# Kernel tuning notes

Measured on AMD Instinct MI355X. Metric: run time of the kernel, lower is better.

The kernel has to match this reference:

```python
import jax, jax.numpy as jnp
import numpy as np

B, N, C, H = 8, 4096, 256, 8
D = C // H
HID = 4 * C
EPS = 1e-5

def _ln(x, w, b):
    mu = jnp.mean(x, axis=-1, keepdims=True)
    var = jnp.var(x, axis=-1, keepdims=True)
    return (x - mu) * jax.lax.rsqrt(var + EPS) * w + b

def setup_inputs() -> dict:
    key = jax.random.key(0)
    ks = jax.random.split(key, 16)
    s = lambda k, shp, scale=0.02: jax.random.normal(k, shp, dtype=jnp.float32) * scale
    return {
        "input_": jax.random.normal(ks[0], (B, N, C), dtype=jnp.float32),
        "prev_state": jax.random.normal(ks[1], (B, N, C), dtype=jnp.float32),
        "pos_embed": jax.random.normal(ks[2], (1, N, C), dtype=jnp.float32),
        "norm1_w": jnp.ones((C,), jnp.float32), "norm1_b": jnp.zeros((C,), jnp.float32),
        "norm2_w": jnp.ones((C,), jnp.float32), "norm2_b": jnp.zeros((C,), jnp.float32),
        "norm3_w": jnp.ones((C,), jnp.float32), "norm3_b": jnp.zeros((C,), jnp.float32),
        "qkv_input_w": s(ks[3], (3 * C, C)),
        "qkv_state_w": s(ks[4], (3 * C, C)),
        "proj_w": s(ks[5], (C, C)), "proj_b": jnp.zeros((C,), jnp.float32),
        "gate_w": s(ks[6], (C, 2 * C)), "gate_b": jnp.zeros((C,), jnp.float32),
        "fc1_w": s(ks[7], (HID, C)), "fc1_b": jnp.zeros((HID,), jnp.float32),
        "fc2_w": s(ks[8], (C, HID)), "fc2_b": jnp.zeros((C,), jnp.float32),
    }

def reference(input_, prev_state, pos_embed,
              norm1_w, norm1_b, norm2_w, norm2_b, norm3_w, norm3_b,
              qkv_input_w, qkv_state_w, proj_w, proj_b,
              gate_w, gate_b, fc1_w, fc1_b, fc2_w, fc2_b):
    input_pos = input_ + pos_embed
    x_ln = _ln(input_pos, norm1_w, norm1_b)
    s_ln = _ln(prev_state, norm2_w, norm2_b)
    # fused QKV from input and state; torch Linear: x @ W.T
    qkv_i = (x_ln @ qkv_input_w.T).reshape(B, N, 3, H, D).transpose(2, 0, 3, 1, 4)
    qkv_s = (s_ln @ qkv_state_w.T).reshape(B, N, 3, H, D).transpose(2, 0, 3, 1, 4)
    q = qkv_i[0] + qkv_s[0]  # [B,H,N,D]
    k = qkv_i[1] + qkv_s[1]
    v = qkv_i[2] + qkv_s[2]
    phi_q = jax.nn.elu(q) + 1.0
    phi_k = jax.nn.elu(k) + 1.0
    # (phi_q @ phi_k^T) @ v reordered associatively to O(N*D^2)
    kv = jnp.einsum('bhnd,bhne->bhde', phi_k, v)        # [B,H,D,D]
    attn = jnp.einsum('bhnd,bhde->bhne', phi_q, kv)     # [B,H,N,D]
    attn = attn.transpose(0, 2, 1, 3).reshape(B, N, C)
    attn = attn @ proj_w.T + proj_b
    output = input_pos + attn
    stacked = jnp.concatenate([input_, prev_state], axis=2)
    update = jax.nn.sigmoid(stacked @ gate_w.T + gate_b)
    new_state = prev_state * (1.0 - update) + attn * update
    h = _ln(output, norm3_w, norm3_b)
    h = jax.nn.gelu(h @ fc1_w.T + fc1_b, approximate=False) @ fc2_w.T + fc2_b
    output = output + h
    return (output, new_state)
```

## Files before the change

### kernel.cpp

```cpp
#include <hip/hip_runtime.h>
#include <cmath>

typedef unsigned short u16;
typedef __attribute__((ext_vector_type(8))) short short8;
typedef __attribute__((ext_vector_type(4))) float f32x4;
typedef __attribute__((ext_vector_type(4))) u16 u16x4;

__device__ __forceinline__ float b2f(u16 u) {
    unsigned x = ((unsigned)u) << 16;
    return __builtin_bit_cast(float, x);
}
__device__ __forceinline__ u16 f2b(float f) {
    unsigned x = __builtin_bit_cast(unsigned, f);
    unsigned r = (x + 0x7fffu + ((x >> 16) & 1u)) >> 16;
    return (u16)r;
}
__device__ __forceinline__ float loadx(const void* p, size_t i, int f32) {
    return f32 ? ((const float*)p)[i] : b2f(((const u16*)p)[i]);
}
__device__ __forceinline__ void stage8f(u16* dst, const void* src, size_t eoff) {
    const f32x4* s = (const f32x4*)((const float*)src + eoff);
    f32x4 a = s[0], b = s[1];
    uint4 p;
    p.x = (unsigned)f2b(a[0]) | ((unsigned)f2b(a[1]) << 16);
    p.y = (unsigned)f2b(a[2]) | ((unsigned)f2b(a[3]) << 16);
    p.z = (unsigned)f2b(b[0]) | ((unsigned)f2b(b[1]) << 16);
    p.w = (unsigned)f2b(b[2]) | ((unsigned)f2b(b[3]) << 16);
    *(uint4*)dst = p;
}
__device__ __forceinline__ void gl_lds16(const void* g, void* l) {
    __builtin_amdgcn_global_load_lds(
        (const __attribute__((address_space(1))) void*)g,
        (__attribute__((address_space(3))) void*)l, 16, 0, 0);
}
__device__ __forceinline__ float gelu_f(float x) {
    float y = 0.7978845608028654f * (x + 0.044715f * x * x * x);
    float e = __expf(2.f * y);
    float t = 1.f - 2.f / (e + 1.f);
    return 0.5f * x * (1.f + t);
}

#define BB 8
#define NN 4096
#define CC 256
#define HH 8
#define DD 32
#define HID 1024
#define MTOK (BB*NN)
#define TOKEL ((size_t)MTOK*CC)

#define WS_INPUT_POS 0u
#define WS_PHIQ   16777216u
#define WS_PHIK   33554432u
#define WS_V      50331648u
#define WS_XLN    67108864u
#define WS_SLN    83886080u
#define WS_OUTPRE 100663296u
#define WS_FLAG   117440512u

__global__ __launch_bounds__(64) void detect_kernel(const u16* __restrict__ in0,
                                                    int* __restrict__ flag)
{
    int t = threadIdx.x;
    u16 w = in0[2 * t];
    int e = (w >> 7) & 0xFF;
    int bad = (e < 64 || e > 192) ? 1 : 0;
    unsigned long long m = __ballot(bad);
    if (t == 0) *flag = (__popcll(m) > 8) ? 1 : 0;
}

__global__ __launch_bounds__(256) void prep_kernel(
    const void* __restrict__ inp, const void* __restrict__ prev,
    const void* __restrict__ pos,
    const void* __restrict__ w1, const void* __restrict__ b1,
    const void* __restrict__ w2, const void* __restrict__ b2,
    u16* __restrict__ input_pos, u16* __restrict__ x_ln, u16* __restrict__ s_ln,
    const int* __restrict__ flagp)
{
    const int f32 = *flagp;
    const int m = blockIdx.x;
    const int c = threadIdx.x;
    const int n = m & (NN - 1);
    const size_t idx = (size_t)m * CC + c;

    __shared__ float red[8];

    float ip = loadx(inp, idx, f32) + loadx(pos, (size_t)n * CC + c, f32);
    float s = ip, s2 = ip * ip;
    #pragma unroll
    for (int o = 32; o; o >>= 1) { s += __shfl_down(s, o, 64); s2 += __shfl_down(s2, o, 64); }
    if ((threadIdx.x & 63) == 0) { int w6 = threadIdx.x >> 6; red[w6] = s; red[4 + w6] = s2; }
    __syncthreads();
    float mu  = (red[0] + red[1] + red[2] + red[3]) * (1.f / 256.f);
    float var = (red[4] + red[5] + red[6] + red[7]) * (1.f / 256.f) - mu * mu;
    float rs = rsqrtf(var + 1e-5f);
    input_pos[idx] = f2b(ip);
    x_ln[idx] = f2b((ip - mu) * rs * loadx(w1, c, f32) + loadx(b1, c, f32));
    __syncthreads();

    float pv = loadx(prev, idx, f32);
    s = pv; s2 = pv * pv;
    #pragma unroll
    for (int o = 32; o; o >>= 1) { s += __shfl_down(s, o, 64); s2 += __shfl_down(s2, o, 64); }
    if ((threadIdx.x & 63) == 0) { int w6 = threadIdx.x >> 6; red[w6] = s; red[4 + w6] = s2; }
    __syncthreads();
    mu  = (red[0] + red[1] + red[2] + red[3]) * (1.f / 256.f);
    var = (red[4] + red[5] + red[6] + red[7]) * (1.f / 256.f) - mu * mu;
    rs = rsqrtf(var + 1e-5f);
    s_ln[idx] = f2b((pv - mu) * rs * loadx(w2, c, f32) + loadx(b2, c, f32));
}

__global__ __launch_bounds__(256) void ln3_kernel(
    const u16* __restrict__ op, const void* __restrict__ w,
    const void* __restrict__ b, u16* __restrict__ out, const int* __restrict__ flagp)
{
    const int f32 = *flagp;
    const size_t m = blockIdx.x;
    const int c = threadIdx.x;
    const size_t idx = m * CC + c;
    __shared__ float red[8];
    float x = b2f(op[idx]);
    float s = x, s2 = x * x;
    #pragma unroll
    for (int o = 32; o; o >>= 1) { s += __shfl_down(s, o, 64); s2 += __shfl_down(s2, o, 64); }
    if ((threadIdx.x & 63) == 0) { int w6 = threadIdx.x >> 6; red[w6] = s; red[4 + w6] = s2; }
    __syncthreads();
    float mu  = (red[0] + red[1] + red[2] + red[3]) * (1.f / 256.f);
    float var = (red[4] + red[5] + red[6] + red[7]) * (1.f / 256.f) - mu * mu;
    out[idx] = f2b((x - mu) * rsqrtf(var + 1e-5f) * loadx(w, c, f32) + loadx(b, c, f32));
}

__global__ __launch_bounds__(64) void kv_mfma(
    const u16* __restrict__ phik_t, const u16* __restrict__ v_t,
    float* __restrict__ kvout)
{
    const int bh = blockIdx.x;
    const int k0 = blockIdx.y * 256;
    const int lane = threadIdx.x;
    const int quad = lane >> 4, lr = lane & 15;

    const u16* A = phik_t + (size_t)bh * DD * NN;
    const u16* W = v_t    + (size_t)bh * DD * NN;

    f32x4 acc[2][2];
    #pragma unroll
    for (int i = 0; i < 2; ++i)
        #pragma unroll
        for (int j = 0; j < 2; ++j) { f32x4 z = {0.f,0.f,0.f,0.f}; acc[i][j] = z; }

    for (int kk = k0; kk < k0 + 256; kk += 32) {
        short8 a0 = *(const short8*)(A + (size_t)lr * NN + kk + quad * 8);
        short8 a1 = *(const short8*)(A + (size_t)(16 + lr) * NN + kk + quad * 8);
        short8 w0 = *(const short8*)(W + (size_t)lr * NN + kk + quad * 8);
        short8 w1 = *(const short8*)(W + (size_t)(16 + lr) * NN + kk + quad * 8);
        acc[0][0] = __builtin_amdgcn_mfma_f32_16x16x32_bf16(a0, w0, acc[0][0], 0, 0, 0);
        acc[0][1] = __builtin_amdgcn_mfma_f32_16x16x32_bf16(a0, w1, acc[0][1], 0, 0, 0);
        acc[1][0] = __builtin_amdgcn_mfma_f32_16x16x32_bf16(a1, w0, acc[1][0], 0, 0, 0);
        acc[1][1] = __builtin_amdgcn_mfma_f32_16x16x32_bf16(a1, w1, acc[1][1], 0, 0, 0);
    }
    float* base = kvout + (size_t)bh * (DD * DD);
    #pragma unroll
    for (int i = 0; i < 2; ++i)
        #pragma unroll
        for (int j = 0; j < 2; ++j)
            #pragma unroll
            for (int r = 0; r < 4; ++r)
                atomicAdd(base + (i * 16 + quad * 4 + r) * DD + j * 16 + lr, acc[i][j][r]);
}

__global__ __launch_bounds__(256) void attn_mfma(
    const u16* __restrict__ phiq, const float* __restrict__ kv,
    u16* __restrict__ attn_tok)
{
    const int bh = blockIdx.x;
    const int b = bh >> 3, h = bh & 7;
    const int wv = threadIdx.x >> 6, lane = threadIdx.x & 63;
    const int quad = lane >> 4, lr = lane & 15;

    const float* kvb = kv + (size_t)bh * (DD * DD);
    short8 bf0, bf1;
    #pragma unroll
    for (int j = 0; j < 8; ++j) {
        int d = quad * 8 + j;
        bf0[j] = (short)f2b(kvb[d * DD + lr]);
        bf1[j] = (short)f2b(kvb[d * DD + 16 + lr]);
    }

    const u16* qb = phiq + (size_t)bh * NN * DD;
    const int n0 = blockIdx.y * 512 + wv * 128;
    #pragma unroll
    for (int t = 0; t < 8; ++t) {
        const int nt = n0 + t * 16;
        short8 af = *(const short8*)(qb + (size_t)(nt + lr) * DD + quad * 8);
        f32x4 c0 = {0.f,0.f,0.f,0.f}, c1 = {0.f,0.f,0.f,0.f};
        c0 = __builtin_amdgcn_mfma_f32_16x16x32_bf16(af, bf0, c0, 0, 0, 0);
        c1 = __builtin_amdgcn_mfma_f32_16x16x32_bf16(af, bf1, c1, 0, 0, 0);
        size_t base = ((size_t)b * NN + nt + quad * 4) * CC + h * DD;
        #pragma unroll
        for (int r = 0; r < 4; ++r) {
            attn_tok[base + (size_t)r * CC + lr]      = f2b(c0[r]);
            attn_tok[base + (size_t)r * CC + 16 + lr] = f2b(c1[r]);
        }
    }
}

#define BM 128
#define BN 128
#define BK 32
#define LDT 32

template <int MODE, int RAWA>
__global__ __launch_bounds__(256) void gemm_bt(
    const void* __restrict__ A1, const void* __restrict__ A2,
    const void* __restrict__ W1, const void* __restrict__ W2,
    int lda, int ldw, int K, int Ksplit, int wcol2,
    const void* __restrict__ bias,
    u16* __restrict__ o0, u16* __restrict__ o1,
    const u16* __restrict__ xa, const void* __restrict__ xr,
    void* __restrict__ oraw, const int* __restrict__ flagp)
{
    __shared__ u16 ash[BM * LDT];
    __shared__ u16 bsh[BN * LDT];

    const int f32 = *flagp;
    const int af32 = RAWA ? f32 : 0;

    const int tid = threadIdx.x;
    const int lane = tid & 63;
    const int wv = tid >> 6;
    const int wm = wv >> 1, wn = wv & 1;
    const int quad = lane >> 4, lr = lane & 15;

    const bool swp = (MODE == 0) ? (blockIdx.x < 2) : true;

    f32x4 acc[4][4];
    #pragma unroll
    for (int i = 0; i < 4; ++i)
        #pragma unroll
        for (int j = 0; j < 4; ++j) { f32x4 z = {0.f,0.f,0.f,0.f}; acc[i][j] = z; }

    const size_t arow0 = (size_t)blockIdx.y * BM;
    const size_t wrow0 = (size_t)blockIdx.x * BN;

    const int srow = lane >> 2;
    const int skc  = (lane & 3) << 3;

    for (int k0 = 0; k0 < K; k0 += BK) {
        const void* As; const void* Ws; int ka, kw;
        if (k0 < Ksplit) { As = A1; Ws = W1; ka = k0;          kw = k0; }
        else             { As = A2; Ws = W2; ka = k0 - Ksplit; kw = k0 - Ksplit + wcol2; }

        if (!af32) {
            const u16* ga = (const u16*)As + (arow0 + wv * 32 + srow) * (size_t)lda + ka + skc;
            u16* la = ash + (wv * 32) * LDT;
            gl_lds16(ga, la);
            gl_lds16(ga + (size_t)16 * lda, la + 16 * LDT);
        } else {
            #pragma unroll
            for (int half = 0; half < 2; ++half) {
                int row = wv * 32 + half * 16 + srow;
                stage8f(ash + row * LDT + skc, As, (arow0 + row) * (size_t)lda + ka + skc);
            }
        }
        if (!f32) {
            const u16* gw = (const u16*)Ws + (wrow0 + wv * 32 + srow) * (size_t)ldw + kw + skc;
            u16* lb = bsh + (wv * 32) * LDT;
            gl_lds16(gw, lb);
            gl_lds16(gw + (size_t)16 * ldw, lb + 16 * LDT);
        } else {
            #pragma unroll
            for (int half = 0; half < 2; ++half) {
                int row = wv * 32 + half * 16 + srow;
                stage8f(bsh + row * LDT + skc, Ws, (wrow0 + row) * (size_t)ldw + kw + skc);
            }
        }
        __syncthreads();

        short8 af[4], bf[4];
        #pragma unroll
        for (int i = 0; i < 4; ++i)
            af[i] = *(const short8*)(ash + (wm * 64 + i * 16 + lr) * LDT + quad * 8);
        #pragma unroll
        for (int j = 0; j < 4; ++j)
            bf[j] = *(const short8*)(bsh + (wn * 64 + j * 16 + lr) * LDT + quad * 8);
        if (swp) {
            #pragma unroll
            for (int i = 0; i < 4; ++i)
                #pragma unroll
                for (int j = 0; j < 4; ++j)
                    acc[i][j] = __builtin_amdgcn_mfma_f32_16x16x32_bf16(bf[j], af[i], acc[i][j], 0, 0, 0);
        } else {
            #pragma unroll
            for (int i = 0; i < 4; ++i)
                #pragma unroll
                for (int j = 0; j < 4; ++j)
                    acc[i][j] = __builtin_amdgcn_mfma_f32_16x16x32_bf16(af[i], bf[j], acc[i][j], 0, 0, 0);
        }
        __syncthreads();
    }

    const int mbase = blockIdx.y * BM + wm * 64;
    const int nbase = blockIdx.x * BN + wn * 64;
    constexpr int LDOUT = (MODE == 3) ? HID : CC;

    #pragma unroll
    for (int i = 0; i < 4; ++i) {
        #pragma unroll
        for (int j = 0; j < 4; ++j) {
            if (MODE == 0) {
                if (swp) {
                    const int m = mbase + i * 16 + lr;
                    const int b = m >> 12, n = m & (NN - 1);
                    const int c0 = nbase + j * 16 + quad * 4;
                    const int h = c0 >> 5, d0 = c0 & 31;
                    u16x4 p;
                    #pragma unroll
                    for (int r = 0; r < 4; ++r) {
                        float v = acc[i][j][r];
                        p[r] = f2b((v > 0.f) ? (v + 1.f) : __expf(v));
                    }
                    *(u16x4*)(o0 + (((size_t)b * HH + h) * NN + n) * DD + d0) = p;
                } else {
                    const int c = nbase + j * 16 + lr;
                    const int which = c >> 8, rem = c & 255, h = rem >> 5, d = rem & 31;
                    const int m0 = mbase + i * 16 + quad * 4;
                    const int b = m0 >> 12, n0i = m0 & (NN - 1);
                    u16x4 p;
                    #pragma unroll
                    for (int r = 0; r < 4; ++r) {
                        float v = acc[i][j][r];
                        if (which == 1) v = (v > 0.f) ? (v + 1.f) : __expf(v);
                        p[r] = f2b(v);
                    }
                    u16* dst = o0 + (size_t)which * TOKEL;
                    *(u16x4*)(dst + (((size_t)b * HH + h) * DD + d) * NN + n0i) = p;
                }
            } else {
                const int m = mbase + i * 16 + lr;
                const int c0 = nbase + j * 16 + quad * 4;
                const size_t idx0 = (size_t)m * LDOUT + c0;
                float bias4[4];
                if (f32) {
                    f32x4 t = *(const f32x4*)((const float*)bias + c0);
                    #pragma unroll
                    for (int r = 0; r < 4; ++r) bias4[r] = t[r];
                } else {
                    u16x4 t = *(const u16x4*)((const u16*)bias + c0);
                    #pragma unroll
                    for (int r = 0; r < 4; ++r) bias4[r] = b2f(t[r]);
                }
                if (MODE == 1) {
                    u16x4 xa4 = *(const u16x4*)(xa + idx0);
                    u16x4 po, pr;
                    #pragma unroll
                    for (int r = 0; r < 4; ++r) {
                        float val = acc[i][j][r] + bias4[r];
                        po[r] = f2b(val);
                        pr[r] = f2b(b2f(xa4[r]) + val);
                    }
                    *(u16x4*)(o0 + idx0) = po;
                    *(u16x4*)(o1 + idx0) = pr;
                } else if (MODE == 2) {
                    u16x4 ap4 = *(const u16x4*)(xa + idx0);
                    float res[4];
                    if (f32) {
                        f32x4 pv = *(const f32x4*)((const float*)xr + idx0);
                        #pragma unroll
                        for (int r = 0; r < 4; ++r) {
                            float u = 1.f / (1.f + __expf(-(acc[i][j][r] + bias4[r])));
                            res[r] = pv[r] * (1.f - u) + b2f(ap4[r]) * u;
                        }
                        f32x4 o; o[0]=res[0]; o[1]=res[1]; o[2]=res[2]; o[3]=res[3];
                        *(f32x4*)((float*)oraw + TOKEL + idx0) = o;
                    } else {
                        u16x4 pv = *(const u16x4*)((const u16*)xr + idx0);
                        u16x4 o;
                        #pragma unroll
                        for (int r = 0; r < 4; ++r) {
                            float u = 1.f / (1.f + __expf(-(acc[i][j][r] + bias4[r])));
                            o[r] = f2b(b2f(pv[r]) * (1.f - u) + b2f(ap4[r]) * u);
                        }
                        *(u16x4*)((u16*)oraw + TOKEL + idx0) = o;
                    }
                } else if (MODE == 3) {
                    u16x4 p;
                    #pragma unroll
                    for (int r = 0; r < 4; ++r)
                        p[r] = f2b(gelu_f(acc[i][j][r] + bias4[r]));
                    *(u16x4*)(o0 + idx0) = p;
                } else {
                    u16x4 xa4 = *(const u16x4*)(xa + idx0);
                    if (f32) {
                        f32x4 o;
                        #pragma unroll
                        for (int r = 0; r < 4; ++r)
                            o[r] = b2f(xa4[r]) + acc[i][j][r] + bias4[r];
                        *(f32x4*)((float*)oraw + idx0) = o;
                    } else {
                        u16x4 o;
                        #pragma unroll
                        for (int r = 0; r < 4; ++r)
                            o[r] = f2b(b2f(xa4[r]) + acc[i][j][r] + bias4[r]);
                        *(u16x4*)((u16*)oraw + idx0) = o;
                    }
                }
            }
        }
    }
}

extern "C" void kernel_launch(void* const* d_in, const int* in_sizes, int n_in,
                              void* d_out, int out_size, void* d_ws, size_t ws_size,
                              hipStream_t stream)
{
    const void* input_ = d_in[0];
    const void* prev   = d_in[1];
    const void* pos    = d_in[2];
    const void* n1w = d_in[3];  const void* n1b = d_in[4];
    const void* n2w = d_in[5];  const void* n2b = d_in[6];
    const void* n3w = d_in[7];  const void* n3b = d_in[8];
    const void* qkvi = d_in[9]; const void* qkvs = d_in[10];
    const void* projw = d_in[11]; const void* projb = d_in[12];
    const void* gatew = d_in[13]; const void* gateb = d_in[14];
    const void* fc1w = d_in[15]; const void* fc1b = d_in[16];
    const void* fc2w = d_in[17]; const void* fc2b = d_in[18];

    char* ws = (char*)d_ws;
    u16* input_pos = (u16*)(ws + WS_INPUT_POS);
    u16* phiq  = (u16*)(ws + WS_PHIQ);
    u16* phikt = (u16*)(ws + WS_PHIK);
    u16* vt    = (u16*)(ws + WS_V);
    u16* x_ln = (u16*)(ws + WS_XLN);
    u16* s_ln = (u16*)(ws + WS_SLN);
    u16* attn_tok = x_ln;
    u16* attn_proj = phikt;
    float* kvf = (float*)(ws + WS_SLN);
    u16* ln3o = s_ln;
    u16* outpre = (u16*)(ws + WS_OUTPRE);
    u16* h1 = (u16*)(ws + WS_INPUT_POS);
    int* flagp = (int*)(ws + WS_FLAG);

    detect_kernel<<<1, 64, 0, stream>>>((const u16*)input_, flagp);
    prep_kernel<<<MTOK, 256, 0, stream>>>(input_, prev, pos, n1w, n1b, n2w, n2b,
                                          input_pos, x_ln, s_ln, flagp);
    gemm_bt<0, 0><<<dim3(3 * CC / BN, MTOK / BM), 256, 0, stream>>>(
        x_ln, s_ln, qkvi, qkvs, CC, CC, 2 * CC, CC, 0, nullptr,
        phiq, nullptr, nullptr, nullptr, nullptr, flagp);
    hipMemsetAsync((void*)kvf, 0, BB * HH * DD * DD * sizeof(float), stream);
    kv_mfma<<<dim3(BB * HH, 16), 64, 0, stream>>>(phikt, vt, kvf);
    attn_mfma<<<dim3(BB * HH, NN / 512), 256, 0, stream>>>(phiq, kvf, attn_tok);
    gemm_bt<1, 0><<<dim3(CC / BN, MTOK / BM), 256, 0, stream>>>(
        attn_tok, attn_tok, projw, projw, CC, CC, CC, CC, 0, projb,
        attn_proj, outpre, input_pos, nullptr, nullptr, flagp);
    gemm_bt<2, 1><<<dim3(CC / BN, MTOK / BM), 256, 0, stream>>>(
        input_, prev, gatew, gatew, CC, 2 * CC, 2 * CC, CC, CC, gateb,
        nullptr, nullptr, attn_proj, prev, d_out, flagp);
    ln3_kernel<<<MTOK, 256, 0, stream>>>(outpre, n3w, n3b, ln3o, flagp);
    gemm_bt<3, 0><<<dim3(HID / BN, MTOK / BM), 256, 0, stream>>>(
        ln3o, ln3o, fc1w, fc1w, CC, CC, CC, CC, 0, fc1b,
        h1, nullptr, nullptr, nullptr, nullptr, flagp);
    gemm_bt<4, 0><<<dim3(CC / BN, MTOK / BM), 256, 0, stream>>>(
        h1, h1, fc2w, fc2w, HID, HID, HID, HID, 0, fc2b,
        nullptr, nullptr, outpre, nullptr, d_out, flagp);
}
```

Measured before the change: 501.2 us.

## Pre-convert weights and raw inputs to bf16, relayout LDS tiles, remap workgroups per XCD

Adds a kernel that converts all weights and biases to bf16 once per call into device globals. The prep kernel now also writes bf16 copies of input and prev_state, so every GEMM, including the gate GEMM, can stage A and W through direct global-to-LDS loads instead of the fp32 convert-and-store path. The LDS tiles move to a k-group-major layout that changes the access pattern for the load and MFMA fragment reads. Workgroup IDs are remapped round-robin across 8 chunks, apparently to keep neighbouring tiles on the same XCD for L2 reuse. The cost is an extra launch and extra bf16 writes of both 8M-element tensors.

```diff
diff --git a/kernel.cpp b/kernel.cpp
--- a/kernel.cpp
+++ b/kernel.cpp
@@ -17,16 +17,6 @@
 }
 __device__ __forceinline__ float loadx(const void* p, size_t i, int f32) {
     return f32 ? ((const float*)p)[i] : b2f(((const u16*)p)[i]);
-}
-__device__ __forceinline__ void stage8f(u16* dst, const void* src, size_t eoff) {
-    const f32x4* s = (const f32x4*)((const float*)src + eoff);
-    f32x4 a = s[0], b = s[1];
-    uint4 p;
-    p.x = (unsigned)f2b(a[0]) | ((unsigned)f2b(a[1]) << 16);
-    p.y = (unsigned)f2b(a[2]) | ((unsigned)f2b(a[3]) << 16);
-    p.z = (unsigned)f2b(b[0]) | ((unsigned)f2b(b[1]) << 16);
-    p.w = (unsigned)f2b(b[2]) | ((unsigned)f2b(b[3]) << 16);
-    *(uint4*)dst = p;
 }
 __device__ __forceinline__ void gl_lds16(const void* g, void* l) {
     __builtin_amdgcn_global_load_lds(
@@ -48,6 +38,7 @@
 #define HID 1024
 #define MTOK (BB*NN)
 #define TOKEL ((size_t)MTOK*CC)
+#define TOKELC 8388608
 
 #define WS_INPUT_POS 0u
 #define WS_PHIQ   16777216u
@@ -58,6 +49,22 @@
 #define WS_OUTPRE 100663296u
 #define WS_FLAG   117440512u
 
+#define OFF_QKVI  0u
+#define OFF_QKVS  196608u
+#define OFF_PROJW 393216u
+#define OFF_GATEW 458752u
+#define OFF_FC1W  589824u
+#define OFF_FC2W  851968u
+#define OFF_PROJB 1114112u
+#define OFF_GATEB 1114368u
+#define OFF_FC1B  1114624u
+#define OFF_FC2B  1115648u
+#define WTOT      1115904u
+
+__device__ __attribute__((aligned(16))) u16 g_wb[WTOT];
+__device__ __attribute__((aligned(16))) u16 g_inb[TOKELC];
+__device__ __attribute__((aligned(16))) u16 g_prevb[TOKELC];
+
 __global__ __launch_bounds__(64) void detect_kernel(const u16* __restrict__ in0,
                                                     int* __restrict__ flag)
 {
@@ -67,6 +74,28 @@
     int bad = (e < 64 || e > 192) ? 1 : 0;
     unsigned long long m = __ballot(bad);
     if (t == 0) *flag = (__popcll(m) > 8) ? 1 : 0;
+}
+
+__global__ __launch_bounds__(256) void wconv_kernel(
+    const void* qkvi, const void* qkvs, const void* projw, const void* gatew,
+    const void* fc1w, const void* fc2w, const void* projb, const void* gateb,
+    const void* fc1b, const void* fc2b, const int* __restrict__ flagp)
+{
+    const int f32 = *flagp;
+    unsigned i = blockIdx.x * 256 + threadIdx.x;
+    if (i >= WTOT) return;
+    const void* src; unsigned off;
+    if      (i < OFF_QKVS)  { src = qkvi;  off = OFF_QKVI; }
+    else if (i < OFF_PROJW) { src = qkvs;  off = OFF_QKVS; }
+    else if (i < OFF_GATEW) { src = projw; off = OFF_PROJW; }
+    else if (i < OFF_FC1W)  { src = gatew; off = OFF_GATEW; }
+    else if (i < OFF_FC2W)  { src = fc1w;  off = OFF_FC1W; }
+    else if (i < OFF_PROJB) { src = fc2w;  off = OFF_FC2W; }
+    else if (i < OFF_GATEB) { src = projb; off = OFF_PROJB; }
+    else if (i < OFF_FC1B)  { src = gateb; off = OFF_GATEB; }
+    else if (i < OFF_FC2B)  { src = fc1b;  off = OFF_FC1B; }
+    else                    { src = fc2b;  off = OFF_FC2B; }
+    g_wb[i] = f2b(loadx(src, i - off, f32));
 }
 
 __global__ __launch_bounds__(256) void prep_kernel(
@@ -85,7 +114,9 @@
 
     __shared__ float red[8];
 
-    float ip = loadx(inp, idx, f32) + loadx(pos, (size_t)n * CC + c, f32);
+    float inr = loadx(inp, idx, f32);
+    float ip = inr + loadx(pos, (size_t)n * CC + c, f32);
+    g_inb[idx] = f2b(inr);
     float s = ip, s2 = ip * ip;
     #pragma unroll
     for (int o = 32; o; o >>= 1) { s += __shfl_down(s, o, 64); s2 += __shfl_down(s2, o, 64); }
@@ -99,6 +130,7 @@
     __syncthreads();
 
     float pv = loadx(prev, idx, f32);
+    g_prevb[idx] = f2b(pv);
     s = pv; s2 = pv * pv;
     #pragma unroll
     for (int o = 32; o; o >>= 1) { s += __shfl_down(s, o, 64); s2 += __shfl_down(s2, o, 64); }
@@ -207,23 +239,36 @@
 #define BM 128
 #define BN 128
 #define BK 32
-#define LDT 32
-
-template <int MODE, int RAWA>
+
+template <int MODE>
 __global__ __launch_bounds__(256) void gemm_bt(
-    const void* __restrict__ A1, const void* __restrict__ A2,
-    const void* __restrict__ W1, const void* __restrict__ W2,
+    const u16* __restrict__ A1in, const u16* __restrict__ A2in,
     int lda, int ldw, int K, int Ksplit, int wcol2,
-    const void* __restrict__ bias,
     u16* __restrict__ o0, u16* __restrict__ o1,
     const u16* __restrict__ xa, const void* __restrict__ xr,
     void* __restrict__ oraw, const int* __restrict__ flagp)
 {
-    __shared__ u16 ash[BM * LDT];
-    __shared__ u16 bsh[BN * LDT];
-
-    const int f32 = *flagp;
-    const int af32 = RAWA ? f32 : 0;
+    __shared__ __attribute__((aligned(16))) u16 ash[BM * BK];
+    __shared__ __attribute__((aligned(16))) u16 bsh[BN * BK];
+
+    const int f32 = (MODE == 2 || MODE == 4) ? *flagp : 0;
+
+    const u16* W1; const u16* W2; const u16* bias = nullptr;
+    if (MODE == 0)      { W1 = g_wb + OFF_QKVI; W2 = g_wb + OFF_QKVS; }
+    else if (MODE == 1) { W1 = W2 = g_wb + OFF_PROJW; bias = g_wb + OFF_PROJB; }
+    else if (MODE == 2) { W1 = W2 = g_wb + OFF_GATEW; bias = g_wb + OFF_GATEB; }
+    else if (MODE == 3) { W1 = W2 = g_wb + OFF_FC1W;  bias = g_wb + OFF_FC1B; }
+    else                { W1 = W2 = g_wb + OFF_FC2W;  bias = g_wb + OFF_FC2B; }
+    const u16* A1 = (MODE == 2) ? g_inb   : A1in;
+    const u16* A2 = (MODE == 2) ? g_prevb : A2in;
+
+    const int gx = gridDim.x;
+    const int nwg = gx * (int)gridDim.y;
+    const int hw = blockIdx.y * gx + blockIdx.x;
+    const int qq = nwg >> 3, rr = nwg & 7;
+    const int xc = hw & 7, pp = hw >> 3;
+    const int nid = (xc < rr ? xc * (qq + 1) : rr * (qq + 1) + (xc - rr) * qq) + pp;
+    const int bx = nid % gx, by = nid / gx;
 
     const int tid = threadIdx.x;
     const int lane = tid & 63;
@@ -231,7 +276,7 @@
     const int wm = wv >> 1, wn = wv & 1;
     const int quad = lane >> 4, lr = lane & 15;
 
-    const bool swp = (MODE == 0) ? (blockIdx.x < 2) : true;
+    const bool swp = (MODE == 0) ? (bx < 2) : true;
 
     f32x4 acc[4][4];
     #pragma unroll
@@ -239,50 +284,38 @@
         #pragma unroll
         for (int j = 0; j < 4; ++j) { f32x4 z = {0.f,0.f,0.f,0.f}; acc[i][j] = z; }
 
-    const size_t arow0 = (size_t)blockIdx.y * BM;
-    const size_t wrow0 = (size_t)blockIdx.x * BN;
-
-    const int srow = lane >> 2;
-    const int skc  = (lane & 3) << 3;
+    const size_t arow0 = (size_t)by * BM;
+    const size_t wrow0 = (size_t)bx * BN;
+
+    const int srow = lane & 31;
+    const int sg   = (lane >> 5) << 3;
 
     for (int k0 = 0; k0 < K; k0 += BK) {
-        const void* As; const void* Ws; int ka, kw;
+        const u16* As; const u16* Ws; int ka, kw;
         if (k0 < Ksplit) { As = A1; Ws = W1; ka = k0;          kw = k0; }
         else             { As = A2; Ws = W2; ka = k0 - Ksplit; kw = k0 - Ksplit + wcol2; }
 
-        if (!af32) {
-            const u16* ga = (const u16*)As + (arow0 + wv * 32 + srow) * (size_t)lda + ka + skc;
-            u16* la = ash + (wv * 32) * LDT;
-            gl_lds16(ga, la);
-            gl_lds16(ga + (size_t)16 * lda, la + 16 * LDT);
-        } else {
-            #pragma unroll
-            for (int half = 0; half < 2; ++half) {
-                int row = wv * 32 + half * 16 + srow;
-                stage8f(ash + row * LDT + skc, As, (arow0 + row) * (size_t)lda + ka + skc);
-            }
+        const u16* ga = As + (arow0 + wv * 32 + srow) * (size_t)lda + ka + sg;
+        u16* la = ash + (wv << 10);
+        gl_lds16(ga, la);
+        gl_lds16(ga + 16, la + 512);
+        const u16* gw = Ws + (wrow0 + wv * 32 + srow) * (size_t)ldw + kw + sg;
+        u16* lb = bsh + (wv << 10);
+        gl_lds16(gw, lb);
+        gl_lds16(gw + 16, lb + 512);
+        __syncthreads();
+
+        short8 af[4], bf[4];
+        #pragma unroll
+        for (int i = 0; i < 4; ++i) {
+            const int ra = wm * 64 + i * 16 + lr;
+            af[i] = *(const short8*)(ash + ((ra >> 5) << 10) + (quad << 8) + ((ra & 31) << 3));
         }
-        if (!f32) {
-            const u16* gw = (const u16*)Ws + (wrow0 + wv * 32 + srow) * (size_t)ldw + kw + skc;
-            u16* lb = bsh + (wv * 32) * LDT;
-            gl_lds16(gw, lb);
-            gl_lds16(gw + (size_t)16 * ldw, lb + 16 * LDT);
-        } else {
-            #pragma unroll
-            for (int half = 0; half < 2; ++half) {
-                int row = wv * 32 + half * 16 + srow;
-                stage8f(bsh + row * LDT + skc, Ws, (wrow0 + row) * (size_t)ldw + kw + skc);
-            }
+        #pragma unroll
+        for (int j = 0; j < 4; ++j) {
+            const int rb = wn * 64 + j * 16 + lr;
+            bf[j] = *(const short8*)(bsh + ((rb >> 5) << 10) + (quad << 8) + ((rb & 31) << 3));
         }
-        __syncthreads();
-
-        short8 af[4], bf[4];
-        #pragma unroll
-        for (int i = 0; i < 4; ++i)
-            af[i] = *(const short8*)(ash + (wm * 64 + i * 16 + lr) * LDT + quad * 8);
-        #pragma unroll
-        for (int j = 0; j < 4; ++j)
-            bf[j] = *(const short8*)(bsh + (wn * 64 + j * 16 + lr) * LDT + quad * 8);
         if (swp) {
             #pragma unroll
             for (int i = 0; i < 4; ++i)
@@ -299,8 +332,8 @@
         __syncthreads();
     }
 
-    const int mbase = blockIdx.y * BM + wm * 64;
-    const int nbase = blockIdx.x * BN + wn * 64;
+    const int mbase = by * BM + wm * 64;
+    const int nbase = bx * BN + wn * 64;
     constexpr int LDOUT = (MODE == 3) ? HID : CC;
 
     #pragma unroll
@@ -340,12 +373,8 @@
                 const int c0 = nbase + j * 16 + quad * 4;
                 const size_t idx0 = (size_t)m * LDOUT + c0;
                 float bias4[4];
-                if (f32) {
-                    f32x4 t = *(const f32x4*)((const float*)bias + c0);
-                    #pragma unroll
-                    for (int r = 0; r < 4; ++r) bias4[r] = t[r];
-                } else {
-                    u16x4 t = *(const u16x4*)((const u16*)bias + c0);
+                {
+                    u16x4 t = *(const u16x4*)(bias + c0);
                     #pragma unroll
                     for (int r = 0; r < 4; ++r) bias4[r] = b2f(t[r]);
                 }
@@ -362,15 +391,14 @@
                     *(u16x4*)(o1 + idx0) = pr;
                 } else if (MODE == 2) {
                     u16x4 ap4 = *(const u16x4*)(xa + idx0);
-                    float res[4];
                     if (f32) {
                         f32x4 pv = *(const f32x4*)((const float*)xr + idx0);
+                        f32x4 o;
                         #pragma unroll
                         for (int r = 0; r < 4; ++r) {
                             float u = 1.f / (1.f + __expf(-(acc[i][j][r] + bias4[r])));
-                            res[r] = pv[r] * (1.f - u) + b2f(ap4[r]) * u;
+                            o[r] = pv[r] * (1.f - u) + b2f(ap4[r]) * u;
                         }
-                        f32x4 o; o[0]=res[0]; o[1]=res[1]; o[2]=res[2]; o[3]=res[3];
                         *(f32x4*)((float*)oraw + TOKEL + idx0) = o;
                     } else {
                         u16x4 pv = *(const u16x4*)((const u16*)xr + idx0);
@@ -441,25 +469,27 @@
     int* flagp = (int*)(ws + WS_FLAG);
 
     detect_kernel<<<1, 64, 0, stream>>>((const u16*)input_, flagp);
+    wconv_kernel<<<(WTOT + 255) / 256, 256, 0, stream>>>(
+        qkvi, qkvs, projw, gatew, fc1w, fc2w, projb, gateb, fc1b, fc2b, flagp);
     prep_kernel<<<MTOK, 256, 0, stream>>>(input_, prev, pos, n1w, n1b, n2w, n2b,
                                           input_pos, x_ln, s_ln, flagp);
-    gemm_bt<0, 0><<<dim3(3 * CC / BN, MTOK / BM), 256, 0, stream>>>(
-        x_ln, s_ln, qkvi, qkvs, CC, CC, 2 * CC, CC, 0, nullptr,
+    gemm_bt<0><<<dim3(3 * CC / BN, MTOK / BM), 256, 0, stream>>>(
+        x_ln, s_ln, CC, CC, 2 * CC, CC, 0,
         phiq, nullptr, nullptr, nullptr, nullptr, flagp);
     hipMemsetAsync((void*)kvf, 0, BB * HH * DD * DD * sizeof(float), stream);
     kv_mfma<<<dim3(BB * HH, 16), 64, 0, stream>>>(phikt, vt, kvf);
     attn_mfma<<<dim3(BB * HH, NN / 512), 256, 0, stream>>>(phiq, kvf, attn_tok);
-    gemm_bt<1, 0><<<dim3(CC / BN, MTOK / BM), 256, 0, stream>>>(
-        attn_tok, attn_tok, projw, projw, CC, CC, CC, CC, 0, projb,
+    gemm_bt<1><<<dim3(CC / BN, MTOK / BM), 256, 0, stream>>>(
+        attn_tok, attn_tok, CC, CC, CC, CC, 0,
         attn_proj, outpre, input_pos, nullptr, nullptr, flagp);
-    gemm_bt<2, 1><<<dim3(CC / BN, MTOK / BM), 256, 0, stream>>>(
-        input_, prev, gatew, gatew, CC, 2 * CC, 2 * CC, CC, CC, gateb,
+    gemm_bt<2><<<dim3(CC / BN, MTOK / BM), 256, 0, stream>>>(
+        nullptr, nullptr, CC, 2 * CC, 2 * CC, CC, CC,
         nullptr, nullptr, attn_proj, prev, d_out, flagp);
     ln3_kernel<<<MTOK, 256, 0, stream>>>(outpre, n3w, n3b, ln3o, flagp);
-    gemm_bt<3, 0><<<dim3(HID / BN, MTOK / BM), 256, 0, stream>>>(
-        ln3o, ln3o, fc1w, fc1w, CC, CC, CC, CC, 0, fc1b,
+    gemm_bt<3><<<dim3(HID / BN, MTOK / BM), 256, 0, stream>>>(
+        ln3o, ln3o, CC, CC, CC, CC, 0,
         h1, nullptr, nullptr, nullptr, nullptr, flagp);
-    gemm_bt<4, 0><<<dim3(CC / BN, MTOK / BM), 256, 0, stream>>>(
-        h1, h1, fc2w, fc2w, HID, HID, HID, HID, 0, fc2b,
+    gemm_bt<4><<<dim3(CC / BN, MTOK / BM), 256, 0, stream>>>(
+        h1, h1, HID, HID, HID, HID, 0,
         nullptr, nullptr, outpre, nullptr, d_out, flagp);
 }
```

Result: faster. 478.2 us (-4.6%).
